# Optimization experiments

Hardware: AMD Instinct MI355X
Metric: run time of the kernel (lower is better)

Reference implementation:

```python
import jax, jax.numpy as jnp
import numpy as np

B, T, D = 2, 2048, 2048
H, G = 16, 4          # query heads, kv groups (GQA)
DK = D // H           # 128
THETA = 10000.0


def _rope(x, pos):
    # x: (B, h, T, dk); half-split rotary embedding
    dk = x.shape[-1]
    inv_freq = 1.0 / (THETA ** (jnp.arange(0, dk // 2, dtype=jnp.float32) * 2.0 / dk))
    ang = pos.astype(jnp.float32)[:, None] * inv_freq[None, :]   # (T, dk/2)
    cos, sin = jnp.cos(ang), jnp.sin(ang)                        # (T, dk/2)
    x1, x2 = x[..., : dk // 2], x[..., dk // 2 :]
    return jnp.concatenate([x1 * cos - x2 * sin, x2 * cos + x1 * sin], axis=-1)


def setup_inputs() -> dict:
    key = jax.random.key(0)
    ks = jax.random.split(key, 5)
    scale = D ** -0.5
    x = jax.random.normal(ks[0], (B, T, D), jnp.float32)
    Wq = jax.random.normal(ks[1], (D, H * DK), jnp.float32) * scale
    Wk = jax.random.normal(ks[2], (D, G * DK), jnp.float32) * scale
    Wv = jax.random.normal(ks[3], (D, G * DK), jnp.float32) * scale
    Wo = jax.random.normal(ks[4], (D, D), jnp.float32) * scale
    mask = jnp.tril(jnp.ones((T, T), dtype=bool))   # causal mask, True = attend
    pos = jnp.arange(T, dtype=jnp.int32)
    return {"x": x, "Wq": Wq, "Wk": Wk, "Wv": Wv, "Wo": Wo, "mask": mask, "pos": pos}


def reference(x, Wq, Wk, Wv, Wo, mask, pos):
    b, t, d = x.shape
    # projections (bias-free linears)
    q = (x @ Wq).reshape(b, t, H, DK).transpose(0, 2, 1, 3)   # (b, h, t, dk)
    k = (x @ Wk).reshape(b, t, G, DK).transpose(0, 2, 1, 3)   # (b, g, t, dk)
    v = (x @ Wv).reshape(b, t, G, DK).transpose(0, 2, 1, 3)
    # RoPE on q and k (module applies rope_q(q,q) and rope_k(k,k))
    q = _rope(q, pos)
    k = _rope(k, pos)
    # GQA: repeat_interleave kv heads to match query heads
    rf = H // G
    k = jnp.repeat(k, rf, axis=1)   # (b, h, t, dk)
    v = jnp.repeat(v, rf, axis=1)
    # scores + causal mask + softmax
    att = jnp.einsum('bhtd,bhTd->bhtT', q, k) / np.float32(np.sqrt(DK))
    att = jnp.where(mask[None, None, :, :], att, -jnp.inf)
    att = jax.nn.softmax(att, axis=-1)
    y = jnp.einsum('bhtT,bhTd->bhtd', att, v)
    y = y.transpose(0, 2, 1, 3).reshape(b, t, d)
    return y @ Wo
```

## Files before the change

### kernel.cpp

```cpp
#include <hip/hip_runtime.h>
#include <cstdint>
#include <cmath>


#define GLOBAL_AS __attribute__((address_space(1)))
#define LDS_AS __attribute__((address_space(3)))

typedef __bf16 bf16x8 __attribute__((ext_vector_type(8)));
typedef __bf16 bf16x4 __attribute__((ext_vector_type(4)));
typedef float f32x4 __attribute__((ext_vector_type(4)));
typedef float f32x16 __attribute__((ext_vector_type(16)));

constexpr int Tn = 2048;

__device__ __forceinline__ f32x4 mfma_bf16(bf16x8 a, bf16x8 b, f32x4 c) {
  return __builtin_amdgcn_mfma_f32_16x16x32_bf16(a, b, c, 0, 0, 0);
}
__device__ __forceinline__ f32x16 mfma32(bf16x8 a, bf16x8 b, f32x16 c) {
  return __builtin_amdgcn_mfma_f32_32x32x16_bf16(a, b, c, 0, 0, 0);
}
__device__ __forceinline__ uint32_t pack_bf16(float a, float b) {
  union { __bf16 h[2]; uint32_t u; } c;
  c.h[0] = (__bf16)a;
  c.h[1] = (__bf16)b;
  return c.u;
}

__global__ __launch_bounds__(256) void convert_f32_bf16(const float* __restrict__ src,
                                                        __bf16* __restrict__ dst,
                                                        size_t n4) {
  const size_t i = (size_t)blockIdx.x * 256 + threadIdx.x;
  if (i >= n4) return;
  const f32x4 v = ((const f32x4*)src)[i];
  bf16x4 o;
#pragma unroll
  for (int k = 0; k < 4; ++k) o[k] = (__bf16)v[k];
  ((bf16x4*)dst)[i] = o;
}

__global__ __launch_bounds__(256) void transpose_f32_bf16(const float* __restrict__ src,
                                                          __bf16* __restrict__ dst,
                                                          int K, int N) {
  __shared__ __bf16 tile[32][33];
  const int n0 = blockIdx.x * 32, k0 = blockIdx.y * 32;
  const int tx = threadIdx.x, ty = threadIdx.y;
#pragma unroll
  for (int i = 0; i < 32; i += 8)
    tile[ty + i][tx] = (__bf16)src[(size_t)(k0 + ty + i) * N + n0 + tx];
  __syncthreads();
#pragma unroll
  for (int i = 0; i < 32; i += 8)
    dst[(size_t)(n0 + ty + i) * K + k0 + tx] = tile[tx][ty + i];
}

__global__ __launch_bounds__(256) void transpose_v(const __bf16* __restrict__ qkv,
                                                   __bf16* __restrict__ vtg) {
  __shared__ __bf16 tile[32][33];
  const int bg = blockIdx.z;
  const int b = bg >> 2, g = bg & 3;
  const int key0 = blockIdx.x * 32, d0 = blockIdx.y * 32;
  const int tx = threadIdx.x, ty = threadIdx.y;
  const __bf16* src = qkv + (size_t)b * Tn * 3072 + 2560 + g * 128;
  __bf16* dst = vtg + (size_t)bg * 128 * Tn;
#pragma unroll
  for (int i = 0; i < 32; i += 8)
    tile[ty + i][tx] = src[(size_t)(key0 + ty + i) * 3072 + d0 + tx];
  __syncthreads();
#pragma unroll
  for (int i = 0; i < 32; i += 8)
    dst[(size_t)(d0 + ty + i) * Tn + key0 + tx] = tile[tx][ty + i];
}

__global__ __launch_bounds__(256, 4) void gemm_bt(const __bf16* __restrict__ A,
                                                  const __bf16* __restrict__ BT,
                                                  void* __restrict__ C,
                                                  int K, int ldc, int outf32) {
  __shared__ __attribute__((aligned(16))) __bf16 As[2][4096];
  __shared__ __attribute__((aligned(16))) __bf16 Bs[2][4096];
  const int tid = threadIdx.x;
  const int wave = tid >> 6, lane = tid & 63;
  const int lr = lane & 15, lq = lane >> 4;
  const int wm = wave >> 1, wn = wave & 1;
  const int m0 = blockIdx.y * 128, n0 = blockIdx.x * 128;

  f32x4 acc[4][4] = {};

  const __bf16* ga[2];
  const __bf16* gb[2];
#pragma unroll
  for (int jj = 0; jj < 2; ++jj) {
    const int j = wave * 2 + jj;
    ga[jj] = A + (size_t)(m0 + j * 16 + lr) * K + lq * 8;
    gb[jj] = BT + (size_t)(n0 + j * 16 + lr) * K + lq * 8;
  }

#pragma unroll
  for (int jj = 0; jj < 2; ++jj) {
    const int j = wave * 2 + jj;
    __builtin_amdgcn_global_load_lds((GLOBAL_AS void*)ga[jj],
                                     (LDS_AS void*)(&As[0][j * 512]), 16, 0, 0);
    __builtin_amdgcn_global_load_lds((GLOBAL_AS void*)gb[jj],
                                     (LDS_AS void*)(&Bs[0][j * 512]), 16, 0, 0);
    ga[jj] += 32;
    gb[jj] += 32;
  }

  int cur = 0;
  for (int kt = 0; kt < K; kt += 32) {
    __syncthreads();
    if (kt + 32 < K) {
#pragma unroll
      for (int jj = 0; jj < 2; ++jj) {
        const int j = wave * 2 + jj;
        __builtin_amdgcn_global_load_lds((GLOBAL_AS void*)ga[jj],
                                         (LDS_AS void*)(&As[cur ^ 1][j * 512]), 16, 0, 0);
        __builtin_amdgcn_global_load_lds((GLOBAL_AS void*)gb[jj],
                                         (LDS_AS void*)(&Bs[cur ^ 1][j * 512]), 16, 0, 0);
        ga[jj] += 32;
        gb[jj] += 32;
      }
    }

    bf16x8 af[4], bfv[4];
#pragma unroll
    for (int i = 0; i < 4; ++i) {
      af[i]  = *(const bf16x8*)(&As[cur][((wm * 4 + i) * 64 + lane) * 8]);
      bfv[i] = *(const bf16x8*)(&Bs[cur][((wn * 4 + i) * 64 + lane) * 8]);
    }
    __builtin_amdgcn_s_setprio(1);
#pragma unroll
    for (int i = 0; i < 4; ++i)
#pragma unroll
      for (int j = 0; j < 4; ++j)
        acc[i][j] = mfma_bf16(af[i], bfv[j], acc[i][j]);
    __builtin_amdgcn_s_setprio(0);
    cur ^= 1;
  }

#pragma unroll
  for (int i = 0; i < 4; ++i) {
    const int row = m0 + wm * 64 + i * 16 + lq * 4;
#pragma unroll
    for (int j = 0; j < 4; ++j) {
      const int col = n0 + wn * 64 + j * 16 + lr;
#pragma unroll
      for (int r = 0; r < 4; ++r) {
        if (outf32)
          ((float*)C)[(size_t)(row + r) * ldc + col] = acc[i][j][r];
        else
          ((__bf16*)C)[(size_t)(row + r) * ldc + col] = (__bf16)acc[i][j][r];
      }
    }
  }
}

__global__ __launch_bounds__(256) void rope_kernel(__bf16* __restrict__ qkv) {
  const int row = blockIdx.x;
  const int t = row & (Tn - 1);
  for (int p = threadIdx.x; p < 1280; p += 256) {
    const int d = p & 63;
    const int hh = p >> 6;
    const int col = (hh < 16) ? (hh * 128 + d) : (2048 + (hh - 16) * 128 + d);
    const float inv = exp2f((float)d * (-13.287712379549449f / 64.f));
    const float ang = (float)t * inv;
    float sn, cs;
    __sincosf(ang, &sn, &cs);
    __bf16* ptr = qkv + (size_t)row * 3072 + col;
    const float x1 = (float)ptr[0];
    const float x2 = (float)ptr[64];
    ptr[0] = (__bf16)(x1 * cs - x2 * sn);
    ptr[64] = (__bf16)(x2 * cs + x1 * sn);
  }
}

constexpr int KVB = 64;
__global__ __launch_bounds__(256, 2) void flash_attn(const __bf16* __restrict__ qkv,
                                                     const __bf16* __restrict__ vtg,
                                                     __bf16* __restrict__ y) {
  const int b = blockIdx.y >> 4, h = blockIdx.y & 15;
  const int g = h >> 2;
  const int q0 = ((int)gridDim.x - 1 - (int)blockIdx.x) * 128;
  const int tid = threadIdx.x;
  const int wave = tid >> 6, lane = tid & 63;
  const int l31 = lane & 31, hi = lane >> 5;

  const __bf16* Qb = qkv + (size_t)b * Tn * 3072 + h * 128;
  const __bf16* Kb = qkv + (size_t)b * Tn * 3072 + 2048 + g * 128;
  const __bf16* Vt = vtg + (size_t)(b * 4 + g) * 128 * Tn;

  __shared__ __attribute__((aligned(16))) __bf16 Ks[2][8192];
  __shared__ __attribute__((aligned(16))) __bf16 Vs[2][8192];

  const __bf16* ksrc[4];
  const __bf16* vsrc[4];
#pragma unroll
  for (int i = 0; i < 4; ++i) {
    ksrc[i] = Kb + (size_t)((i >> 1) * 32 + l31) * 3072 + ((i * 4 + wave) & 7) * 16 + hi * 8;
    vsrc[i] = Vt + (size_t)(i * 32 + l31) * Tn + wave * 16 + hi * 8;
  }

  const int qg = q0 + wave * 32 + l31;
  bf16x8 qf[8];
#pragma unroll
  for (int s = 0; s < 8; ++s)
    qf[s] = *(const bf16x8*)(Qb + (size_t)qg * 3072 + s * 16 + hi * 8);

  f32x16 o[4] = {};
  float m_i = -1e30f, l_i = 0.f;
  const float kscale = 0.12752909695983215f;

#pragma unroll
  for (int i = 0; i < 4; ++i) {
    __builtin_amdgcn_global_load_lds((GLOBAL_AS void*)ksrc[i],
                                     (LDS_AS void*)(&Ks[0][(i * 256 + wave * 64) * 8]), 16, 0, 0);
    __builtin_amdgcn_global_load_lds((GLOBAL_AS void*)vsrc[i],
                                     (LDS_AS void*)(&Vs[0][(i * 256 + wave * 64) * 8]), 16, 0, 0);
    ksrc[i] += (size_t)KVB * 3072;
    vsrc[i] += KVB;
  }
  __syncthreads();

  const int ktend = q0 + 128;
  int cur = 0;
  for (int kt = 0; kt < ktend; kt += KVB) {
    if (kt + KVB < ktend) {
#pragma unroll
      for (int i = 0; i < 4; ++i) {
        __builtin_amdgcn_global_load_lds(
            (GLOBAL_AS void*)ksrc[i],
            (LDS_AS void*)(&Ks[cur ^ 1][(i * 256 + wave * 64) * 8]), 16, 0, 0);
        __builtin_amdgcn_global_load_lds(
            (GLOBAL_AS void*)vsrc[i],
            (LDS_AS void*)(&Vs[cur ^ 1][(i * 256 + wave * 64) * 8]), 16, 0, 0);
        ksrc[i] += (size_t)KVB * 3072;
        vsrc[i] += KVB;
      }
    }

    if (kt <= q0 + wave * 32 + 31) {
      f32x16 sa[2] = {};
      __builtin_amdgcn_s_setprio(1);
#pragma unroll
      for (int kb = 0; kb < 2; ++kb)
#pragma unroll
        for (int s = 0; s < 8; ++s) {
          const bf16x8 kf = *(const bf16x8*)(&Ks[cur][((kb * 8 + s) * 64 + lane) * 8]);
          sa[kb] = mfma32(kf, qf[s], sa[kb]);
        }
      __builtin_amdgcn_s_setprio(0);

      const bool full = (kt + KVB - 1) <= (q0 + wave * 32);
      float mx = -1e30f;
      if (full) {
#pragma unroll
        for (int kb = 0; kb < 2; ++kb)
#pragma unroll
          for (int r = 0; r < 16; ++r) {
            const float v = sa[kb][r] * kscale;
            sa[kb][r] = v;
            mx = fmaxf(mx, v);
          }
      } else {
#pragma unroll
        for (int kb = 0; kb < 2; ++kb)
#pragma unroll
          for (int r = 0; r < 16; ++r) {
            const int key = kt + kb * 32 + (r & 3) + 8 * (r >> 2) + 4 * hi;
            const float v = (key <= qg) ? sa[kb][r] * kscale : -1e30f;
            sa[kb][r] = v;
            mx = fmaxf(mx, v);
          }
      }
      mx = fmaxf(mx, __shfl_xor(mx, 32));
      if (__any(mx > m_i + 8.f)) {
        const float mnew = fmaxf(m_i, mx);
        const float alpha = __builtin_amdgcn_exp2f(m_i - mnew);
        m_i = mnew;
        l_i *= alpha;
#pragma unroll
        for (int db = 0; db < 4; ++db)
#pragma unroll
          for (int r = 0; r < 16; ++r) o[db][r] *= alpha;
      }
      float ls = 0.f;
#pragma unroll
      for (int kb = 0; kb < 2; ++kb)
#pragma unroll
        for (int r = 0; r < 16; ++r) {
          const float pv = __builtin_amdgcn_exp2f(sa[kb][r] - m_i);
          sa[kb][r] = pv;
          ls += pv;
        }
      l_i += ls;

      uint32_t P[2][8], X[2][8];
#pragma unroll
      for (int kb = 0; kb < 2; ++kb)
#pragma unroll
        for (int gg = 0; gg < 8; ++gg)
          P[kb][gg] = pack_bf16(sa[kb][2 * gg], sa[kb][2 * gg + 1]);
#pragma unroll
      for (int kb = 0; kb < 2; ++kb)
#pragma unroll
        for (int gg = 0; gg < 8; ++gg)
          X[kb][gg] = (uint32_t)__shfl_xor((int)P[kb][gg], 32);

      union FU { uint32_t u[4]; bf16x8 v; };
      bf16x8 pf[4];
#pragma unroll
      for (int kb = 0; kb < 2; ++kb) {
        FU f0, f1;
        f0.u[0] = hi ? X[kb][2] : P[kb][0];
        f0.u[1] = hi ? X[kb][3] : P[kb][1];
        f0.u[2] = hi ? P[kb][2] : X[kb][0];
        f0.u[3] = hi ? P[kb][3] : X[kb][1];
        f1.u[0] = hi ? X[kb][6] : P[kb][4];
        f1.u[1] = hi ? X[kb][7] : P[kb][5];
        f1.u[2] = hi ? P[kb][6] : X[kb][4];
        f1.u[3] = hi ? P[kb][7] : X[kb][5];
        pf[kb * 2 + 0] = f0.v;
        pf[kb * 2 + 1] = f1.v;
      }

      __builtin_amdgcn_s_setprio(1);
#pragma unroll
      for (int db = 0; db < 4; ++db)
#pragma unroll
        for (int s = 0; s < 4; ++s) {
          const bf16x8 vf = *(const bf16x8*)(&Vs[cur][((db * 4 + s) * 64 + lane) * 8]);
          o[db] = mfma32(vf, pf[s], o[db]);
        }
      __builtin_amdgcn_s_setprio(0);
    }

    __syncthreads();
    cur ^= 1;
  }

  {
    const float lt = l_i + __shfl_xor(l_i, 32);
    const float inv = 1.0f / lt;
    __bf16* yrow = y + (size_t)(b * Tn + qg) * 2048 + h * 128;
#pragma unroll
    for (int db = 0; db < 4; ++db)
#pragma unroll
      for (int g2 = 0; g2 < 4; ++g2) {
        bf16x4 ov;
#pragma unroll
        for (int j = 0; j < 4; ++j) ov[j] = (__bf16)(o[db][4 * g2 + j] * inv);
        *(bf16x4*)(yrow + db * 32 + 8 * g2 + 4 * hi) = ov;
      }
  }
}

extern "C" void kernel_launch(void* const* d_in, const int* in_sizes, int n_in,
                              void* d_out, int out_size, void* d_ws, size_t ws_size,
                              hipStream_t stream) {
  (void)in_sizes; (void)n_in; (void)out_size; (void)ws_size;
  const float* x  = (const float*)d_in[0];
  const float* Wq = (const float*)d_in[1];
  const float* Wk = (const float*)d_in[2];
  const float* Wv = (const float*)d_in[3];
  const float* Wo = (const float*)d_in[4];
  float* out = (float*)d_out;

  __bf16* xb  = (__bf16*)d_ws;
  __bf16* y   = xb;
  __bf16* WT  = xb + (size_t)4096 * 2048;
  __bf16* WoT = WT;
  __bf16* VtG = WT + (size_t)2048 * 2048;
  __bf16* qkv = WT + (size_t)3072 * 2048;

  convert_f32_bf16<<<(4096 * 2048 / 4 + 255) / 256, 256, 0, stream>>>(x, xb, 4096 * 2048 / 4);
  dim3 tb(32, 8);
  transpose_f32_bf16<<<dim3(64, 64), tb, 0, stream>>>(Wq, WT, 2048, 2048);
  transpose_f32_bf16<<<dim3(16, 64), tb, 0, stream>>>(Wk, WT + (size_t)2048 * 2048, 2048, 512);
  transpose_f32_bf16<<<dim3(16, 64), tb, 0, stream>>>(Wv, WT + (size_t)2560 * 2048, 2048, 512);

  gemm_bt<<<dim3(3072 / 128, 4096 / 128), 256, 0, stream>>>(xb, WT, qkv, 2048, 3072, 0);
  rope_kernel<<<4096, 256, 0, stream>>>(qkv);

  transpose_v<<<dim3(Tn / 32, 4, 8), tb, 0, stream>>>(qkv, VtG);
  transpose_f32_bf16<<<dim3(64, 64), tb, 0, stream>>>(Wo, WoT, 2048, 2048);

  flash_attn<<<dim3(Tn / 128, 2 * 16), 256, 0, stream>>>(qkv, VtG, y);
  gemm_bt<<<dim3(2048 / 128, 4096 / 128), 256, 0, stream>>>(y, WoT, out, 2048, 2048, 1);
}
```

Measured before the change: 402.0 us.

## Triple-buffer GEMM LDS tiles with explicit vmcnt waits for deeper prefetch

The bf16 GEMM moves from double to triple LDS buffering. It prefetches two k-tiles ahead and waits with s_waitcnt vmcnt(4) rather than draining all loads at each syncthreads. The aim is to hide global-to-LDS latency behind MFMA work. In exchange, LDS per block grows from 32KB to 48KB, which may limit occupancy against launch_bounds(256,4), and correctness depends on the hand-counted outstanding loads.

```diff
diff --git a/kernel.cpp b/kernel.cpp
--- a/kernel.cpp
+++ b/kernel.cpp
@@ -75,8 +75,8 @@
                                                   const __bf16* __restrict__ BT,
                                                   void* __restrict__ C,
                                                   int K, int ldc, int outf32) {
-  __shared__ __attribute__((aligned(16))) __bf16 As[2][4096];
-  __shared__ __attribute__((aligned(16))) __bf16 Bs[2][4096];
+  __shared__ __attribute__((aligned(16))) __bf16 As[3][4096];
+  __shared__ __attribute__((aligned(16))) __bf16 Bs[3][4096];
   const int tid = threadIdx.x;
   const int wave = tid >> 6, lane = tid & 63;
   const int lr = lane & 15, lq = lane >> 4;
@@ -95,27 +95,37 @@
   }
 
 #pragma unroll
-  for (int jj = 0; jj < 2; ++jj) {
-    const int j = wave * 2 + jj;
-    __builtin_amdgcn_global_load_lds((GLOBAL_AS void*)ga[jj],
-                                     (LDS_AS void*)(&As[0][j * 512]), 16, 0, 0);
-    __builtin_amdgcn_global_load_lds((GLOBAL_AS void*)gb[jj],
-                                     (LDS_AS void*)(&Bs[0][j * 512]), 16, 0, 0);
-    ga[jj] += 32;
-    gb[jj] += 32;
-  }
-
-  int cur = 0;
-  for (int kt = 0; kt < K; kt += 32) {
-    __syncthreads();
-    if (kt + 32 < K) {
+  for (int s = 0; s < 2; ++s) {
+#pragma unroll
+    for (int jj = 0; jj < 2; ++jj) {
+      const int j = wave * 2 + jj;
+      __builtin_amdgcn_global_load_lds((GLOBAL_AS void*)ga[jj],
+                                       (LDS_AS void*)(&As[s][j * 512]), 16, 0, 0);
+      __builtin_amdgcn_global_load_lds((GLOBAL_AS void*)gb[jj],
+                                       (LDS_AS void*)(&Bs[s][j * 512]), 16, 0, 0);
+      ga[jj] += 32;
+      gb[jj] += 32;
+    }
+  }
+
+  const int nstep = K >> 5;
+  int rd = 0, wr = 2;
+  for (int t = 0; t < nstep; ++t) {
+    if (t + 1 < nstep)
+      asm volatile("s_waitcnt vmcnt(4)" ::: "memory");
+    else
+      asm volatile("s_waitcnt vmcnt(0)" ::: "memory");
+    __builtin_amdgcn_s_barrier();
+    __builtin_amdgcn_sched_barrier(0);
+
+    if (t + 2 < nstep) {
 #pragma unroll
       for (int jj = 0; jj < 2; ++jj) {
         const int j = wave * 2 + jj;
         __builtin_amdgcn_global_load_lds((GLOBAL_AS void*)ga[jj],
-                                         (LDS_AS void*)(&As[cur ^ 1][j * 512]), 16, 0, 0);
+                                         (LDS_AS void*)(&As[wr][j * 512]), 16, 0, 0);
         __builtin_amdgcn_global_load_lds((GLOBAL_AS void*)gb[jj],
-                                         (LDS_AS void*)(&Bs[cur ^ 1][j * 512]), 16, 0, 0);
+                                         (LDS_AS void*)(&Bs[wr][j * 512]), 16, 0, 0);
         ga[jj] += 32;
         gb[jj] += 32;
       }
@@ -124,8 +134,8 @@
     bf16x8 af[4], bfv[4];
 #pragma unroll
     for (int i = 0; i < 4; ++i) {
-      af[i]  = *(const bf16x8*)(&As[cur][((wm * 4 + i) * 64 + lane) * 8]);
-      bfv[i] = *(const bf16x8*)(&Bs[cur][((wn * 4 + i) * 64 + lane) * 8]);
+      af[i]  = *(const bf16x8*)(&As[rd][((wm * 4 + i) * 64 + lane) * 8]);
+      bfv[i] = *(const bf16x8*)(&Bs[rd][((wn * 4 + i) * 64 + lane) * 8]);
     }
     __builtin_amdgcn_s_setprio(1);
 #pragma unroll
@@ -134,7 +144,9 @@
       for (int j = 0; j < 4; ++j)
         acc[i][j] = mfma_bf16(af[i], bfv[j], acc[i][j]);
     __builtin_amdgcn_s_setprio(0);
-    cur ^= 1;
+
+    rd = (rd == 2) ? 0 : rd + 1;
+    wr = (wr == 2) ? 0 : wr + 1;
   }
 
 #pragma unroll
```

Result: no change. 405.7 us (+0.9%).
